# Performance work log

Measured on AMD Instinct MI355X. Metric: run time of the kernel, lower is better.

Reference implementation:

```python
import jax, jax.numpy as jnp
import numpy as np

INPUT_DIM = 246
HIDDEN = 512
OUTPUT_DIM = 123
B, T = 128, 500
N_DIFF, N_ABIL = 11, 8


def setup_inputs() -> dict:
    key = jax.random.key(0)
    ks = jax.random.split(key, 9)
    feats = jax.random.normal(ks[0], (B, T, INPUT_DIM), dtype=jnp.float32)
    ability = jax.random.randint(ks[1], (B, T, 1), 0, N_ABIL).astype(jnp.float32)
    diff = jax.random.randint(ks[2], (B, T, 1), 0, N_DIFF).astype(jnp.float32)
    x = jnp.concatenate([feats, ability, diff], axis=-1)  # [B,T,248]
    in_dim = INPUT_DIM + N_DIFF + N_ABIL  # 265
    s_ih = 1.0 / np.sqrt(HIDDEN)
    W_ih = jax.random.uniform(ks[3], (4 * HIDDEN, in_dim), jnp.float32, -s_ih, s_ih)
    W_hh = jax.random.uniform(ks[4], (4 * HIDDEN, HIDDEN), jnp.float32, -s_ih, s_ih)
    b_ih = jax.random.uniform(ks[5], (4 * HIDDEN,), jnp.float32, -s_ih, s_ih)
    b_hh = jax.random.uniform(ks[6], (4 * HIDDEN,), jnp.float32, -s_ih, s_ih)
    s_fc = 1.0 / np.sqrt(HIDDEN)
    W_fc = jax.random.uniform(ks[7], (OUTPUT_DIM, HIDDEN), jnp.float32, -s_fc, s_fc)
    b_fc = jax.random.uniform(ks[8], (OUTPUT_DIM,), jnp.float32, -s_fc, s_fc)
    return {"x": x, "W_ih": W_ih, "W_hh": W_hh, "b_ih": b_ih, "b_hh": b_hh,
            "W_fc": W_fc, "b_fc": b_fc}


def _lstm(x, W_ih, W_hh, b_ih, b_hh):
    # x: [B,T,In] -> out: [B,T,H]; PyTorch gate order i,f,g,o
    Bsz = x.shape[0]
    H = W_hh.shape[1]
    x_proj = jnp.einsum('bti,gi->btg', x, W_ih) + b_ih + b_hh  # [B,T,4H]

    def step(carry, xt):
        h, c = carry
        gates = xt + h @ W_hh.T
        i, f, g, o = jnp.split(gates, 4, axis=-1)
        i, f, o = jax.nn.sigmoid(i), jax.nn.sigmoid(f), jax.nn.sigmoid(o)
        g = jnp.tanh(g)
        c = f * c + i * g
        h = o * jnp.tanh(c)
        return (h, c), h

    h0 = jnp.zeros((Bsz, H), x.dtype)
    c0 = jnp.zeros((Bsz, H), x.dtype)
    (_, _), hs = jax.lax.scan(step, (h0, c0), x_proj.transpose(1, 0, 2))
    return hs.transpose(1, 0, 2)


def reference(x, W_ih, W_hh, b_ih, b_hh, W_fc, b_fc):
    feats = x[..., :INPUT_DIM]
    ability = x[..., -2].astype(jnp.int32)
    diff = x[..., -1].astype(jnp.int32)
    one_hot_diff = jax.nn.one_hot(diff, N_DIFF, dtype=x.dtype)
    one_hot_ab = jax.nn.one_hot(ability, N_ABIL, dtype=x.dtype)
    new_x = jnp.tanh(jnp.concatenate([feats, one_hot_diff, one_hot_ab], axis=-1))
    out = _lstm(new_x, W_ih, W_hh, b_ih, b_hh)  # [B,T,H]
    res = jax.nn.sigmoid(jnp.einsum('bth,oh->bto', out, W_fc) + b_fc)
    return res[:, :-1, :]
```

## Files before the change

kernel.cpp:

```cpp
#include <hip/hip_runtime.h>
#include <hip/hip_fp16.h>


typedef _Float16 f16;
typedef _Float16 f16x8 __attribute__((ext_vector_type(8)));
typedef float f32x4 __attribute__((ext_vector_type(4)));
typedef unsigned u32x4 __attribute__((ext_vector_type(4)));

#define TS 499

#define NEWX_OFF   0ul
#define NEWX_BYTES (500ul*8*9216)
#define HALL_OFF   (NEWX_OFF + NEWX_BYTES)
#define HALL_BYTES (500ul*128*512*2)
#define WHH_OFF    (HALL_OFF + HALL_BYTES)
#define WHH_BYTES  (2048ul*512*2)
#define WIH_OFF    (WHH_OFF + WHH_BYTES)
#define WIH_BYTES  (2048ul*288*2)
#define WFC_OFF    (WIH_OFF + WIH_BYTES)
#define WFC_BYTES  (128ul*512*2)
#define BIAS_OFF   (WFC_OFF + WFC_BYTES)
#define BIAS_BYTES (2048ul*4)
#define WS_NEED    (BIAS_OFF + BIAS_BYTES)

__device__ __forceinline__ float tanh_dev(float x) {
    float ax = fabsf(x);
    float e  = __expf(-2.f * ax);
    float r  = (1.f - e) / (1.f + e);
    return copysignf(r, x);
}
__device__ __forceinline__ float sigm_dev(float x) {
    float e = __expf(-fabsf(x));
    float p = 1.f / (1.f + e);
    return x >= 0.f ? p : 1.f - p;
}

__global__ void __launch_bounds__(256) prep_newx(const float* __restrict__ x,
                                                 f16* __restrict__ newx) {
    const int t  = blockIdx.x;
    const int bt = blockIdx.y;
    const int tid = threadIdx.x;
    char* tb = (char*)newx + ((size_t)t * 8 + bt) * 9216;
    for (int idx = tid; idx < 16 * 288; idx += 256) {
        const int r = idx / 288, k = idx - r * 288;
        const float* xr = x + ((size_t)(bt * 16 + r) * 500 + t) * 248;
        float v;
        if (k < 246)      v = tanh_dev(xr[k]);
        else if (k < 257) v = (k - 246 == (int)xr[247]) ? 0.76159415595576485f : 0.f;
        else if (k < 265) v = (k - 257 == (int)xr[246]) ? 0.76159415595576485f : 0.f;
        else              v = 0.f;
        const int col8 = k >> 3;
        const int byte = (col8 >> 2) * 1024 + (((col8 & 3) * 16 + r) << 4) + ((k & 7) << 1);
        *(f16*)(tb + byte) = (f16)v;
    }
}

__global__ void __launch_bounds__(256) prep_w(const float* __restrict__ W_ih,
                                              const float* __restrict__ W_hh,
                                              const float* __restrict__ W_fc,
                                              const float* __restrict__ b_ih,
                                              const float* __restrict__ b_hh,
                                              f16* __restrict__ whh, f16* __restrict__ wih,
                                              f16* __restrict__ wfc, float* __restrict__ bias) {
    const int NHH = 2048 * 512;
    const int NIH = 2048 * 288;
    const int NFC = 128 * 512;
    const int NT  = NHH + NIH + NFC + 2048;
    for (int i = blockIdx.x * 256 + threadIdx.x; i < NT; i += gridDim.x * 256) {
        if (i < NHH) {
            whh[i] = (f16)W_hh[i];
        } else if (i < NHH + NIH) {
            int j2 = i - NHH; int rr = j2 / 288, kk = j2 % 288;
            wih[j2] = (kk < 265) ? (f16)W_ih[rr * 265 + kk] : (f16)0.f;
        } else if (i < NHH + NIH + NFC) {
            int j2 = i - (NHH + NIH); int rr = j2 >> 9, kk = j2 & 511;
            wfc[j2] = (rr < 123) ? (f16)W_fc[rr * 512 + kk] : (f16)0.f;
        } else {
            int j2 = i - (NHH + NIH + NFC);
            bias[j2] = b_ih[j2] + b_hh[j2];
        }
    }
}

#define CHKU16(H) { u32x4 _u = __builtin_bit_cast(u32x4, H);                  \
    bad |= (unsigned)((_u[0] >> 16) == 0xFFFFu) | (unsigned)((_u[0] & 0xFFFFu) == 0xFFFFu); \
    bad |= (unsigned)((_u[1] >> 16) == 0xFFFFu) | (unsigned)((_u[1] & 0xFFFFu) == 0xFFFFu); \
    bad |= (unsigned)((_u[2] >> 16) == 0xFFFFu) | (unsigned)((_u[2] & 0xFFFFu) == 0xFFFFu); \
    bad |= (unsigned)((_u[3] >> 16) == 0xFFFFu) | (unsigned)((_u[3] & 0xFFFFu) == 0xFFFFu); }

__device__ __forceinline__ u32x4 scrub(u32x4 h) {
    u32x4 u = h;
    #pragma unroll
    for (int i = 0; i < 4; ++i) {
        unsigned v = u[i];
        if ((v & 0xFFFFu) == 0xFFFFu) v &= 0xFFFF0000u;
        if ((v >> 16)     == 0xFFFFu) v &= 0x0000FFFFu;
        u[i] = v;
    }
    return u;
}

__global__ void __launch_bounds__(512, 1) lstm_seq(const f16* __restrict__ newx_,
                                                   f16* __restrict__ hall,
                                                   const f16* __restrict__ whh,
                                                   const f16* __restrict__ wih,
                                                   const float* __restrict__ bias) {
    __shared__ __align__(16) char hsb[16 * 1024];
    __shared__ float gf[4 * 560];
    __shared__ __align__(16) f16 hout[512];

    const char* newx = (const char*)newx_;
    const int tid = threadIdx.x, bid = blockIdx.x;
    const int btile = bid & 7;
    const int hsl   = bid >> 3;

    const int w = tid >> 6, wl = tid & 63;
    const int arow = wl & 15, kgrp = wl >> 4;
    const int g = w & 3, cb = w >> 2;
    const int grow = g * 512 + hsl * 32 + cb * 16 + arow;
    const int bE = tid >> 5, colE = tid & 31;

    f16x8 wh[16], wi[9];
    #pragma unroll
    for (int kc = 0; kc < 16; ++kc)
        wh[kc] = *(const f16x8*)(whh + (size_t)grow * 512 + kc * 32 + kgrp * 8);
    #pragma unroll
    for (int kc = 0; kc < 9; ++kc)
        wi[kc] = *(const f16x8*)(wih + (size_t)grow * 288 + kc * 32 + kgrp * 8);
    const float bb = bias[grow];

    const int srow = tid & 15, sc8 = tid >> 4;
    const int soff1 = (sc8 >> 2) * 1024 + (((sc8 & 3) * 16 + srow) << 4);
    const int soff2 = soff1 + 8 * 1024;

    float c_st = 0.f;

    f16x8 xa[9];
    {
        const char* xt = newx + (size_t)btile * 9216;
        #pragma unroll
        for (int kc = 0; kc < 9; ++kc)
            xa[kc] = *(const f16x8*)(xt + kc * 1024 + wl * 16);
    }

    for (int t = 0; t < TS; ++t) {
        f32x4 acc = {bb, bb, bb, bb};
        #pragma unroll
        for (int kc = 0; kc < 9; ++kc)
            acc = __builtin_amdgcn_mfma_f32_16x16x32_f16(xa[kc], wi[kc], acc, 0, 0, 0);
        {
            const char* xt1 = newx + ((size_t)(t + 1) * 8 + btile) * 9216;
            #pragma unroll
            for (int kc = 0; kc < 9; ++kc)
                xa[kc] = *(const f16x8*)(xt1 + kc * 1024 + wl * 16);
        }

        if (t > 0) {
            const char* hb = (const char*)hall + ((size_t)(t - 1) * 128 + btile * 16) * 1024;
            const char* ga1 = hb + srow * 1024 + sc8 * 16;
            const char* ga2 = ga1 + 512;
            u32x4 h0, h1;
            int spins = 0;
            bool timeout = false;
            for (;;) {
                asm volatile("global_load_dwordx4 %0, %2, off sc0 sc1\n\t"
                             "global_load_dwordx4 %1, %3, off sc0 sc1\n\t"
                             "s_waitcnt vmcnt(0)"
                             : "=&v"(h0), "=&v"(h1) : "v"(ga1), "v"(ga2) : "memory");
                unsigned bad = 0;
                CHKU16(h0); CHKU16(h1);
                if (__ballot(bad) == 0ull) break;
                if (++spins > 4096) { timeout = true; break; }
                if (spins > 4) __builtin_amdgcn_s_sleep(1);
            }
            if (timeout) { h0 = scrub(h0); h1 = scrub(h1); }
            *(u32x4*)(hsb + soff1) = h0;
            *(u32x4*)(hsb + soff2) = h1;
            __syncthreads();

            f32x4 e0 = {0.f,0.f,0.f,0.f}, e1 = {0.f,0.f,0.f,0.f};
            #pragma unroll
            for (int kc = 0; kc < 16; kc += 2) {
                f16x8 a0 = *(const f16x8*)(hsb + kc * 1024 + wl * 16);
                f16x8 a1 = *(const f16x8*)(hsb + (kc + 1) * 1024 + wl * 16);
                e0 = __builtin_amdgcn_mfma_f32_16x16x32_f16(a0, wh[kc],     e0, 0, 0, 0);
                e1 = __builtin_amdgcn_mfma_f32_16x16x32_f16(a1, wh[kc + 1], e1, 0, 0, 0);
            }
            acc += e0; acc += e1;
        }

        {
            float* gp = gf + g * 560 + cb * 16 + (wl & 15);
            const int b4 = (wl >> 4) * 4;
            gp[(b4 + 0) * 35] = acc[0];
            gp[(b4 + 1) * 35] = acc[1];
            gp[(b4 + 2) * 35] = acc[2];
            gp[(b4 + 3) * 35] = acc[3];
        }
        __syncthreads();

        {
            const float* gq = gf + bE * 35 + colE;
            float iv = sigm_dev(gq[0]);
            float fv = sigm_dev(gq[560]);
            float gv = tanh_dev(gq[1120]);
            float ov = sigm_dev(gq[1680]);
            c_st = fv * c_st + iv * gv;
            float hv = ov * tanh_dev(c_st);
            hout[bE * 32 + colE] = (f16)hv;
        }
        __syncthreads();

        if ((tid >> 6) == (t & 7)) {
            u32x4 hv4 = *(const u32x4*)((const char*)hout + wl * 16);
            const f16* sp = hall + ((size_t)t * 128 + btile * 16 + (wl >> 2)) * 512
                            + hsl * 32 + (wl & 3) * 8;
            asm volatile("global_store_dwordx4 %0, %1, off sc0 sc1"
                         :: "v"(sp), "v"(hv4) : "memory");
        }
    }
}

__global__ void __launch_bounds__(256) out_gemm(const f16* __restrict__ hall,
                                                const f16* __restrict__ wfc,
                                                const float* __restrict__ bfc,
                                                float* __restrict__ out) {
    const int tid = threadIdx.x;
    const int w = tid >> 6, wl = tid & 63;
    const int arow = wl & 15, kgrp = wl >> 4;
    const long m0 = (long)blockIdx.x * 64 + w * 16;
    const f16* ap = hall + (m0 + arow) * 512 + kgrp * 8;
    f16x8 a[16];
    #pragma unroll
    for (int kc = 0; kc < 16; ++kc) a[kc] = *(const f16x8*)(ap + kc * 32);
    #pragma unroll
    for (int jt = 0; jt < 8; ++jt) {
        f32x4 acc = {0.f, 0.f, 0.f, 0.f};
        const f16* bp = wfc + (size_t)(jt * 16 + arow) * 512 + kgrp * 8;
        #pragma unroll
        for (int kc = 0; kc < 16; ++kc)
            acc = __builtin_amdgcn_mfma_f32_16x16x32_f16(a[kc], *(const f16x8*)(bp + kc * 32),
                                                         acc, 0, 0, 0);
        const int col = jt * 16 + arow;
        if (col < 123) {
            const float bv = bfc[col];
            #pragma unroll
            for (int rr = 0; rr < 4; ++rr) {
                long m = m0 + kgrp * 4 + rr;
                int tt = (int)(m >> 7), b = (int)(m & 127);
                out[((size_t)b * 499 + tt) * 123 + col] = sigm_dev(acc[rr] + bv);
            }
        }
    }
}

extern "C" void kernel_launch(void* const* d_in, const int* in_sizes, int n_in,
                              void* d_out, int out_size, void* d_ws, size_t ws_size,
                              hipStream_t stream) {
    if (ws_size < WS_NEED) return;

    const float* x    = (const float*)d_in[0];
    const float* W_ih = (const float*)d_in[1];
    const float* W_hh = (const float*)d_in[2];
    const float* b_ih = (const float*)d_in[3];
    const float* b_hh = (const float*)d_in[4];
    const float* W_fc = (const float*)d_in[5];
    const float* b_fc = (const float*)d_in[6];
    float* out = (float*)d_out;
    char* ws = (char*)d_ws;

    f16* newx   = (f16*)(ws + NEWX_OFF);
    f16* hall   = (f16*)(ws + HALL_OFF);
    f16* whh    = (f16*)(ws + WHH_OFF);
    f16* wih    = (f16*)(ws + WIH_OFF);
    f16* wfc    = (f16*)(ws + WFC_OFF);
    float* bias = (float*)(ws + BIAS_OFF);

    (void)hipMemsetAsync(hall, 0xFF, HALL_BYTES, stream);

    prep_newx<<<dim3(TS, 8), 256, 0, stream>>>(x, newx);
    prep_w<<<512, 256, 0, stream>>>(W_ih, W_hh, W_fc, b_ih, b_hh, whh, wih, wfc, bias);

    lstm_seq<<<dim3(128), dim3(512), 0, stream>>>(newx, hall, whh, wih, bias);

    out_gemm<<<998, 256, 0, stream>>>(hall, wfc, b_fc, out);
}
```

Before: 1.260 ms.

## Fuse output projection into LSTM kernel via consumer blocks polling hidden states

Launches 128 extra blocks in the recurrent kernel that poll the hidden-state buffer (sentinel 0xFFFF fill) for each timestep and compute the FC plus sigmoid output as soon as it is ready, replacing the separate out_gemm launch. This overlaps the output GEMM with the sequential recurrence and removes its tail time. It depends on all 256 blocks being co-resident, and a timeout path scrubs sentinel values if polling stalls. The extra polling traffic may also interfere with the latency-critical recurrent blocks.

```diff
diff --git a/kernel.cpp b/kernel.cpp
--- a/kernel.cpp
+++ b/kernel.cpp
@@ -104,13 +104,92 @@
                                                    f16* __restrict__ hall,
                                                    const f16* __restrict__ whh,
                                                    const f16* __restrict__ wih,
-                                                   const float* __restrict__ bias) {
+                                                   const float* __restrict__ bias,
+                                                   const f16* __restrict__ wfc,
+                                                   const float* __restrict__ bfc,
+                                                   float* __restrict__ out) {
+    const int tid = threadIdx.x, bid = blockIdx.x;
+
+    if (bid >= 128) {
+        const int j = bid - 128;
+        const int w = tid >> 6, wl = tid & 63;
+        const int half = w >> 2, w4 = w & 3;
+        const int arow = wl & 15, kgrp = wl >> 4;
+        for (int tt = j; tt < TS; tt += 128) {
+            const long m0 = (long)tt * 128 + half * 64 + w4 * 16;
+            const char* ap = (const char*)(hall + (m0 + arow) * 512 + kgrp * 8);
+            f16x8 a00,a01,a02,a03,a04,a05,a06,a07,a08,a09,a10,a11,a12,a13,a14,a15;
+            int spins = 0;
+            bool timeout = false;
+            for (;;) {
+                asm volatile(
+                    "global_load_dwordx4 %0,  %16, off sc0 sc1\n\t"
+                    "global_load_dwordx4 %1,  %16, off offset:64 sc0 sc1\n\t"
+                    "global_load_dwordx4 %2,  %16, off offset:128 sc0 sc1\n\t"
+                    "global_load_dwordx4 %3,  %16, off offset:192 sc0 sc1\n\t"
+                    "global_load_dwordx4 %4,  %16, off offset:256 sc0 sc1\n\t"
+                    "global_load_dwordx4 %5,  %16, off offset:320 sc0 sc1\n\t"
+                    "global_load_dwordx4 %6,  %16, off offset:384 sc0 sc1\n\t"
+                    "global_load_dwordx4 %7,  %16, off offset:448 sc0 sc1\n\t"
+                    "global_load_dwordx4 %8,  %16, off offset:512 sc0 sc1\n\t"
+                    "global_load_dwordx4 %9,  %16, off offset:576 sc0 sc1\n\t"
+                    "global_load_dwordx4 %10, %16, off offset:640 sc0 sc1\n\t"
+                    "global_load_dwordx4 %11, %16, off offset:704 sc0 sc1\n\t"
+                    "global_load_dwordx4 %12, %16, off offset:768 sc0 sc1\n\t"
+                    "global_load_dwordx4 %13, %16, off offset:832 sc0 sc1\n\t"
+                    "global_load_dwordx4 %14, %16, off offset:896 sc0 sc1\n\t"
+                    "global_load_dwordx4 %15, %16, off offset:960 sc0 sc1\n\t"
+                    "s_waitcnt vmcnt(0)"
+                    : "=&v"(a00), "=&v"(a01), "=&v"(a02), "=&v"(a03),
+                      "=&v"(a04), "=&v"(a05), "=&v"(a06), "=&v"(a07),
+                      "=&v"(a08), "=&v"(a09), "=&v"(a10), "=&v"(a11),
+                      "=&v"(a12), "=&v"(a13), "=&v"(a14), "=&v"(a15)
+                    : "v"(ap) : "memory");
+                unsigned bad = 0;
+                { u32x4 h;
+                  h = __builtin_bit_cast(u32x4, a00); CHKU16(__builtin_bit_cast(f16x8, h));
+                  h = __builtin_bit_cast(u32x4, a15); CHKU16(__builtin_bit_cast(f16x8, h)); }
+                CHKU16(a01); CHKU16(a02); CHKU16(a03); CHKU16(a04); CHKU16(a05);
+                CHKU16(a06); CHKU16(a07); CHKU16(a08); CHKU16(a09); CHKU16(a10);
+                CHKU16(a11); CHKU16(a12); CHKU16(a13); CHKU16(a14);
+                if (__ballot(bad) == 0ull) break;
+                if (++spins > (1 << 14)) { timeout = true; break; }
+                __builtin_amdgcn_s_sleep(16);
+            }
+            if (timeout) {
+                u32x4 u;
+                u = scrub(__builtin_bit_cast(u32x4, a00)); a00 = __builtin_bit_cast(f16x8, u);
+                u = scrub(__builtin_bit_cast(u32x4, a15)); a15 = __builtin_bit_cast(f16x8, u);
+            }
+            f16x8 a[16] = {a00,a01,a02,a03,a04,a05,a06,a07,a08,a09,a10,a11,a12,a13,a14,a15};
+            #pragma unroll
+            for (int jt = 0; jt < 8; ++jt) {
+                f32x4 acc = {0.f, 0.f, 0.f, 0.f};
+                const f16* bp = wfc + (size_t)(jt * 16 + arow) * 512 + kgrp * 8;
+                #pragma unroll
+                for (int kc = 0; kc < 16; ++kc)
+                    acc = __builtin_amdgcn_mfma_f32_16x16x32_f16(
+                              a[kc], *(const f16x8*)(bp + kc * 32), acc, 0, 0, 0);
+                const int col = jt * 16 + arow;
+                if (col < 123) {
+                    const float bv = bfc[col];
+                    #pragma unroll
+                    for (int rr = 0; rr < 4; ++rr) {
+                        long m = m0 + kgrp * 4 + rr;
+                        int t2 = (int)(m >> 7), b = (int)(m & 127);
+                        out[((size_t)b * 499 + t2) * 123 + col] = sigm_dev(acc[rr] + bv);
+                    }
+                }
+            }
+        }
+        return;
+    }
+
     __shared__ __align__(16) char hsb[16 * 1024];
     __shared__ float gf[4 * 560];
     __shared__ __align__(16) f16 hout[512];
 
     const char* newx = (const char*)newx_;
-    const int tid = threadIdx.x, bid = blockIdx.x;
     const int btile = bid & 7;
     const int hsl   = bid >> 3;
 
@@ -221,39 +300,6 @@
     }
 }
 
-__global__ void __launch_bounds__(256) out_gemm(const f16* __restrict__ hall,
-                                                const f16* __restrict__ wfc,
-                                                const float* __restrict__ bfc,
-                                                float* __restrict__ out) {
-    const int tid = threadIdx.x;
-    const int w = tid >> 6, wl = tid & 63;
-    const int arow = wl & 15, kgrp = wl >> 4;
-    const long m0 = (long)blockIdx.x * 64 + w * 16;
-    const f16* ap = hall + (m0 + arow) * 512 + kgrp * 8;
-    f16x8 a[16];
-    #pragma unroll
-    for (int kc = 0; kc < 16; ++kc) a[kc] = *(const f16x8*)(ap + kc * 32);
-    #pragma unroll
-    for (int jt = 0; jt < 8; ++jt) {
-        f32x4 acc = {0.f, 0.f, 0.f, 0.f};
-        const f16* bp = wfc + (size_t)(jt * 16 + arow) * 512 + kgrp * 8;
-        #pragma unroll
-        for (int kc = 0; kc < 16; ++kc)
-            acc = __builtin_amdgcn_mfma_f32_16x16x32_f16(a[kc], *(const f16x8*)(bp + kc * 32),
-                                                         acc, 0, 0, 0);
-        const int col = jt * 16 + arow;
-        if (col < 123) {
-            const float bv = bfc[col];
-            #pragma unroll
-            for (int rr = 0; rr < 4; ++rr) {
-                long m = m0 + kgrp * 4 + rr;
-                int tt = (int)(m >> 7), b = (int)(m & 127);
-                out[((size_t)b * 499 + tt) * 123 + col] = sigm_dev(acc[rr] + bv);
-            }
-        }
-    }
-}
-
 extern "C" void kernel_launch(void* const* d_in, const int* in_sizes, int n_in,
                               void* d_out, int out_size, void* d_ws, size_t ws_size,
                               hipStream_t stream) {
@@ -281,7 +327,6 @@
     prep_newx<<<dim3(TS, 8), 256, 0, stream>>>(x, newx);
     prep_w<<<512, 256, 0, stream>>>(W_ih, W_hh, W_fc, b_ih, b_hh, whh, wih, wfc, bias);
 
-    lstm_seq<<<dim3(128), dim3(512), 0, stream>>>(newx, hall, whh, wih, bias);
-
-    out_gemm<<<998, 256, 0, stream>>>(hall, wfc, b_fc, out);
-}
+    lstm_seq<<<dim3(256), dim3(512), 0, stream>>>(newx, hall, whh, wih, bias,
+                                                  wfc, b_fc, out);
+}
```

Result: no change. 1.254 ms (-0.5%).
